# Kernel tuning notes

Measured on AMD Instinct MI355X. Metric: run time of the kernel, lower is better.

Reference implementation:

```python
import jax, jax.numpy as jnp
import numpy as np

B, T, M, D, L = 8, 4096, 32768, 128, 3  # L = ebm_GNN_layer_num - 1


def _lin(x, W, b):
    return x @ W + b


def setup_inputs() -> dict:
    key = jax.random.key(0)
    ks = jax.random.split(key, 24)
    s = 0.05
    inp = {
        "x_1st": jax.random.normal(ks[0], (B, T, 2, D), dtype=jnp.float32),
        "x_2nd": jax.random.normal(ks[1], (B, M, 4, D), dtype=jnp.float32),
        "A_causal": jax.random.uniform(ks[2], (B, 1, M), dtype=jnp.float32),
        "edge": jax.random.randint(ks[3], (2, M), 0, T, dtype=jnp.int64),
        # per-layer node/edge weights (stacked over L layers)
        "node_W": jax.random.normal(ks[4], (L, D, D)) * s,
        "node_b": jnp.zeros((L, D)),
        "mlp_W": jax.random.normal(ks[5], (L, D, D)) * s,
        "mlp_b": jnp.zeros((L, D)),
        "edgeL_W": jax.random.normal(ks[6], (L, D, D)) * s,
        "edgeL_b": jnp.zeros((L, D)),
        # node readout MLP: D -> 2D -> D -> 1
        "nro_W1": jax.random.normal(ks[7], (D, 2 * D)) * s, "nro_b1": jnp.zeros((2 * D,)),
        "nro_W2": jax.random.normal(ks[8], (2 * D, D)) * s, "nro_b2": jnp.zeros((D,)),
        "nro_W3": jax.random.normal(ks[9], (D, 1)) * s, "nro_b3": jnp.zeros((1,)),
        # edge readout MLP
        "ero_W1": jax.random.normal(ks[10], (D, 2 * D)) * s, "ero_b1": jnp.zeros((2 * D,)),
        "ero_W2": jax.random.normal(ks[11], (2 * D, D)) * s, "ero_b2": jnp.zeros((D,)),
        "ero_W3": jax.random.normal(ks[12], (D, 1)) * s, "ero_b3": jnp.zeros((1,)),
    }
    return inp


def reference(x_1st, x_2nd, A_causal, node_W, node_b, mlp_W, mlp_b,
              edgeL_W, edgeL_b, nro_W1, nro_b1, nro_W2, nro_b2, nro_W3, nro_b3,
              ero_W1, ero_b1, ero_W2, ero_b2, ero_W3, ero_b3, edge):
    ni = jnp.array([0, 0, 1, 1])  # node_i_indice
    nj = jnp.array([0, 1, 0, 1])  # node_j_indice
    e0, e1 = edge[0], edge[1]
    a = A_causal[:, 0, :, None, None]  # (B, M, 1, 1)
    xn, xe = x_1st, x_2nd
    for i in range(L):
        # --- node layer: gather -> mask-multiply -> scatter_add -> linear ---
        msg = xn[:, e1] * a                          # (B, M, 2, D)
        upd = jnp.zeros_like(xn).at[:, e0].add(msg)  # (B, T, 2, D)
        xn_new = _lin(xn + upd, node_W[i], node_b[i])
        # --- edge layer (uses updated node features, as in torch forward) ---
        ei = xn_new[:, e0][:, :, ni]                 # (B, M, 4, D)
        ej = xn_new[:, e1][:, :, nj]                 # (B, M, 4, D)
        xe_new = _lin(xe + _lin(ei + ej, mlp_W[i], mlp_b[i]), edgeL_W[i], edgeL_b[i])
        if i < L - 1:
            xn_new = jax.nn.relu(xn_new)
            xe_new = jax.nn.relu(xe_new)
        xn, xe = xn_new, xe_new
    # readouts (dropout=0, concat=False)
    h_node = _lin(jax.nn.relu(_lin(jax.nn.relu(_lin(xn, nro_W1, nro_b1)), nro_W2, nro_b2)), nro_W3, nro_b3)[..., 0]
    h_edge = _lin(jax.nn.relu(_lin(jax.nn.relu(_lin(xe, ero_W1, ero_b1)), ero_W2, ero_b2)), ero_W3, ero_b3)[..., 0]
    return h_node, h_edge  # (B,T,2), (B,M,4)
```

## Files before the change

kernel.cpp:

```cpp
#include <hip/hip_runtime.h>

#define NB 8
#define NT 4096
#define NM 32768
#define ND 128

typedef __attribute__((ext_vector_type(8))) short bf16x8;
typedef __attribute__((ext_vector_type(4))) float f32x4;
typedef __attribute__((ext_vector_type(4))) unsigned int u32x4;

#define MFMA(a,b,c) __builtin_amdgcn_mfma_f32_16x16x32_bf16(a,b,c,0,0,0)

__device__ __forceinline__ unsigned short f2bf(float x) {
  unsigned u = __float_as_uint(x);
  u += 0x7FFFu + ((u >> 16) & 1u);
  return (unsigned short)(u >> 16);
}
__device__ __forceinline__ float bf2f(unsigned short h) {
  return __uint_as_float(((unsigned)h) << 16);
}

__device__ __forceinline__ bf16x8 ldsFrag(const char* lds, int row, int kByte, int rowStride) {
  return *(const bf16x8*)(lds + ((row * rowStride + kByte) ^ ((row & 7) << 4)));
}

__global__ __launch_bounds__(256) void k_prep(
    const float* __restrict__ W, char* __restrict__ dst,
    int K, int N, int khShift, int perShift, int total)
{
  int i = blockIdx.x * 256 + threadIdx.x;
  if (i >= total) return;
  int m  = i >> perShift;
  int j  = i & ((1 << perShift) - 1);
  int n  = j >> khShift;
  int kh = j & ((1 << khShift) - 1);
  int k0 = kh << 3;
  const float* Wm = W + (size_t)m * K * N;
  char* dm = dst + (size_t)m * K * N * 2;
  unsigned short tmp[8];
  #pragma unroll
  for (int jj = 0; jj < 8; ++jj) tmp[jj] = f2bf(Wm[(k0 + jj) * N + n]);
  *(u32x4*)(dm + ((n * K * 2 + k0 * 2) ^ ((n & 7) << 4))) = *(u32x4*)tmp;
}

__global__ __launch_bounds__(256) void k_csr_count(const int* __restrict__ edge, int* deg) {
  int m = blockIdx.x * 256 + threadIdx.x;
  if (m < NM) atomicAdd(&deg[edge[m]], 1);
}
__global__ __launch_bounds__(64) void k_csr_scan(const int* __restrict__ deg,
                                                 int* __restrict__ off, int* __restrict__ cursor) {
  __shared__ int partial[64];
  int t = threadIdx.x;
  int base = t * 64;
  int sum = 0;
  for (int i = 0; i < 64; ++i) sum += deg[base + i];
  partial[t] = sum;
  __syncthreads();
  if (t == 0) {
    int run = 0;
    for (int i = 0; i < 64; ++i) { int v = partial[i]; partial[i] = run; run += v; }
  }
  __syncthreads();
  int run = partial[t];
  for (int i = 0; i < 64; ++i) {
    off[base + i] = run; cursor[base + i] = run;
    run += deg[base + i];
  }
  if (t == 63) off[NT] = NM;
}
__global__ __launch_bounds__(256) void k_csr_fill(const int* __restrict__ edge,
                                                  int* cursor, int* __restrict__ csr) {
  int m = blockIdx.x * 256 + threadIdx.x;
  if (m < NM) { int pos = atomicAdd(&cursor[edge[m]], 1); csr[pos] = m; }
}
__global__ __launch_bounds__(256) void k_csr_sort(const int* __restrict__ off, int* __restrict__ csr) {
  int n = blockIdx.x * 256 + threadIdx.x;
  if (n < NT) {
    int s = off[n], e = off[n + 1];
    for (int i = s + 1; i < e; ++i) {
      int v = csr[i]; int j = i - 1;
      while (j >= s && csr[j] > v) { csr[j + 1] = csr[j]; --j; }
      csr[j + 1] = v;
    }
  }
}

__global__ __launch_bounds__(256) void k_node(
    const float* __restrict__ xnIn, float* __restrict__ xnOut,
    const float* __restrict__ A, const int* __restrict__ edge,
    const int* __restrict__ off, const int* __restrict__ csr,
    const float* __restrict__ W, const float* __restrict__ bias, int doReluIn)
{
  __shared__ float Ws[ND * ND];
  __shared__ float xs[32][ND];
  const int t = threadIdx.x;
  for (int i = t; i < ND * ND; i += 256) Ws[i] = W[i];

  const int rowBase = blockIdx.x << 5;
  {
    const int r  = t >> 3;
    const int c0 = (t & 7) << 4;
    const int grow = rowBase + r;
    const int ch   = grow & 1;
    const int node = (grow >> 1) & (NT - 1);
    const int b    = grow >> 13;
    f32x4 acc[4];
    {
      const float4* xr = (const float4*)(xnIn + (size_t)grow * ND + c0);
      #pragma unroll
      for (int q = 0; q < 4; ++q) {
        float4 v = xr[q];
        if (doReluIn) {
          v.x = fmaxf(v.x, 0.f); v.y = fmaxf(v.y, 0.f);
          v.z = fmaxf(v.z, 0.f); v.w = fmaxf(v.w, 0.f);
        }
        acc[q] = (f32x4){v.x, v.y, v.z, v.w};
      }
    }
    const int s = off[node], e = off[node + 1];
    for (int p = s; p < e; ++p) {
      int m = csr[p];
      float a = A[b * NM + m];
      int e1 = edge[NM + m];
      const float4* src = (const float4*)(xnIn + (size_t)(((b * NT + e1) << 1) + ch) * ND + c0);
      #pragma unroll
      for (int q = 0; q < 4; ++q) {
        float4 v = src[q];
        if (doReluIn) {
          v.x = fmaxf(v.x, 0.f); v.y = fmaxf(v.y, 0.f);
          v.z = fmaxf(v.z, 0.f); v.w = fmaxf(v.w, 0.f);
        }
        acc[q][0] = fmaf(a, v.x, acc[q][0]);
        acc[q][1] = fmaf(a, v.y, acc[q][1]);
        acc[q][2] = fmaf(a, v.z, acc[q][2]);
        acc[q][3] = fmaf(a, v.w, acc[q][3]);
      }
    }
    #pragma unroll
    for (int q = 0; q < 4; ++q) *(f32x4*)&xs[r][c0 + q * 4] = acc[q];
  }
  const int c4 = (t & 31) << 2;
  const int rg = t >> 5;
  float4 bv = *(const float4*)(bias + c4);
  __syncthreads();
  float acc[4][4];
  #pragma unroll
  for (int r = 0; r < 4; ++r)
    #pragma unroll
    for (int c = 0; c < 4; ++c) acc[r][c] = 0.f;
  for (int k = 0; k < ND; k += 4) {
    float4 sv[4];
    #pragma unroll
    for (int r = 0; r < 4; ++r) sv[r] = *(const float4*)&xs[(rg << 2) + r][k];
    #pragma unroll
    for (int j = 0; j < 4; ++j) {
      float4 w = *(const float4*)&Ws[(k + j) * ND + c4];
      #pragma unroll
      for (int r = 0; r < 4; ++r) {
        float s = ((const float*)&sv[r])[j];
        acc[r][0] += s * w.x; acc[r][1] += s * w.y;
        acc[r][2] += s * w.z; acc[r][3] += s * w.w;
      }
    }
  }
  #pragma unroll
  for (int r = 0; r < 4; ++r) {
    float4 o;
    o.x = acc[r][0] + bv.x; o.y = acc[r][1] + bv.y;
    o.z = acc[r][2] + bv.z; o.w = acc[r][3] + bv.w;
    *(float4*)&xnOut[(size_t)(rowBase + (rg << 2) + r) * ND + c4] = o;
  }
}

template<int IN_F32>
__global__ __launch_bounds__(512, 4) void k_edge_mfma(
    const float* __restrict__ xn,
    const float* __restrict__ xeInF, const unsigned short* __restrict__ xeInH,
    unsigned short* xeOut,
    const int* __restrict__ edge,
    const char* __restrict__ WmImg, const float* __restrict__ bm,
    const char* __restrict__ WeImg, const float* __restrict__ be,
    int doReluOut, int nTiles)
{
  __shared__ __align__(16) char WmT[128 * 256];
  __shared__ __align__(16) char WeT[128 * 256];
  __shared__ __align__(16) char sA[64 * 256];
  const int t = threadIdx.x;
  {
    const u32x4* sm = (const u32x4*)WmImg;
    const u32x4* se = (const u32x4*)WeImg;
    u32x4* dm = (u32x4*)WmT;
    u32x4* de = (u32x4*)WeT;
    for (int i = t; i < 2048; i += 512) { dm[i] = sm[i]; de[i] = se[i]; }
  }
  const int w   = t >> 6;
  const int l   = t & 63;
  const int l15 = l & 15;
  const int lg  = l >> 4;
  const int rg2 = w >> 2;
  const int wc  = w & 3;
  float bmv[2], bev[2];
  #pragma unroll
  for (int fc = 0; fc < 2; ++fc) {
    int col = wc * 32 + fc * 16 + l15;
    bmv[fc] = bm[col];
    bev[fc] = be[col];
  }
  const int srow = t >> 3;
  __syncthreads();

  for (int tile = blockIdx.x; tile < nTiles; tile += gridDim.x) {
    const int rowBase = tile << 6;
    {
      int grow = rowBase + srow;
      int cch = grow & 3;
      int m = (grow >> 2) & (NM - 1);
      int b = grow >> 17;
      int e0 = edge[m], e1 = edge[NM + m];
      const float4* p0 = (const float4*)(xn + (size_t)((b * NT + e0) * 2 + (cch >> 1)) * ND);
      const float4* p1 = (const float4*)(xn + (size_t)((b * NT + e1) * 2 + (cch & 1)) * ND);
      #pragma unroll
      for (int hh = 0; hh < 2; ++hh) {
        int h = (t & 7) + hh * 8;
        float4 a0 = p0[h * 2], a1 = p0[h * 2 + 1];
        float4 c0 = p1[h * 2], c1 = p1[h * 2 + 1];
        unsigned short tmp[8];
        tmp[0] = f2bf(a0.x + c0.x); tmp[1] = f2bf(a0.y + c0.y);
        tmp[2] = f2bf(a0.z + c0.z); tmp[3] = f2bf(a0.w + c0.w);
        tmp[4] = f2bf(a1.x + c1.x); tmp[5] = f2bf(a1.y + c1.y);
        tmp[6] = f2bf(a1.z + c1.z); tmp[7] = f2bf(a1.w + c1.w);
        *(u32x4*)(sA + ((srow * 256 + h * 16) ^ ((srow & 7) << 4))) = *(u32x4*)tmp;
      }
    }
    float xev[2][2][4];
    #pragma unroll
    for (int fr = 0; fr < 2; ++fr)
      #pragma unroll
      for (int fc = 0; fc < 2; ++fc) {
        int col = wc * 32 + fc * 16 + l15;
        #pragma unroll
        for (int i = 0; i < 4; ++i) {
          int r = rg2 * 32 + fr * 16 + lg * 4 + i;
          size_t idx = (size_t)(rowBase + r) * ND + col;
          xev[fr][fc][i] = IN_F32 ? xeInF[idx] : bf2f(xeInH[idx]);
        }
      }
    __syncthreads();
    f32x4 acc[2][2];
    #pragma unroll
    for (int fr = 0; fr < 2; ++fr)
      #pragma unroll
      for (int fc = 0; fc < 2; ++fc) acc[fr][fc] = (f32x4){0.f, 0.f, 0.f, 0.f};
    #pragma unroll
    for (int ks = 0; ks < 4; ++ks) {
      int kb = ks * 64 + lg * 16;
      bf16x8 b0 = ldsFrag(WmT, wc * 32 + l15,      kb, 256);
      bf16x8 b1 = ldsFrag(WmT, wc * 32 + 16 + l15, kb, 256);
      #pragma unroll
      for (int fr = 0; fr < 2; ++fr) {
        bf16x8 a = ldsFrag(sA, rg2 * 32 + fr * 16 + l15, kb, 256);
        acc[fr][0] = MFMA(a, b0, acc[fr][0]);
        acc[fr][1] = MFMA(a, b1, acc[fr][1]);
      }
    }
    __syncthreads();
    #pragma unroll
    for (int fr = 0; fr < 2; ++fr)
      #pragma unroll
      for (int fc = 0; fc < 2; ++fc) {
        int col = wc * 32 + fc * 16 + l15;
        #pragma unroll
        for (int i = 0; i < 4; ++i) {
          int r = rg2 * 32 + fr * 16 + lg * 4 + i;
          float v = xev[fr][fc][i] + acc[fr][fc][i] + bmv[fc];
          *(unsigned short*)(sA + ((r * 256 + col * 2) ^ ((r & 7) << 4))) = f2bf(v);
        }
      }
    __syncthreads();
    #pragma unroll
    for (int fr = 0; fr < 2; ++fr)
      #pragma unroll
      for (int fc = 0; fc < 2; ++fc) acc[fr][fc] = (f32x4){0.f, 0.f, 0.f, 0.f};
    #pragma unroll
    for (int ks = 0; ks < 4; ++ks) {
      int kb = ks * 64 + lg * 16;
      bf16x8 b0 = ldsFrag(WeT, wc * 32 + l15,      kb, 256);
      bf16x8 b1 = ldsFrag(WeT, wc * 32 + 16 + l15, kb, 256);
      #pragma unroll
      for (int fr = 0; fr < 2; ++fr) {
        bf16x8 a = ldsFrag(sA, rg2 * 32 + fr * 16 + l15, kb, 256);
        acc[fr][0] = MFMA(a, b0, acc[fr][0]);
        acc[fr][1] = MFMA(a, b1, acc[fr][1]);
      }
    }
    __syncthreads();
    #pragma unroll
    for (int fr = 0; fr < 2; ++fr)
      #pragma unroll
      for (int fc = 0; fc < 2; ++fc) {
        int col = wc * 32 + fc * 16 + l15;
        #pragma unroll
        for (int i = 0; i < 4; ++i) {
          int r = rg2 * 32 + fr * 16 + lg * 4 + i;
          float o = acc[fr][fc][i] + bev[fc];
          if (doReluOut) o = fmaxf(o, 0.f);
          xeOut[(size_t)(rowBase + r) * ND + col] = f2bf(o);
        }
      }
  }
}

template<int INBF16>
__global__ __launch_bounds__(512, 2) void k_ro_fused(
    const float* __restrict__ inF, const unsigned short* __restrict__ inH,
    float* __restrict__ out, int nTiles,
    const char* __restrict__ W1Img, const float* __restrict__ b1,
    const char* __restrict__ W2Img, const float* __restrict__ b2,
    const float* __restrict__ W3, const float* __restrict__ b3)
{
  __shared__ __align__(16) char W1T[256 * 256];
  __shared__ __align__(16) char W2T[128 * 512];
  __shared__ __align__(16) char sA[32 * 256];
  __shared__ __align__(16) char h1[32 * 512];
  __shared__ float red[2][32][8];
  const int t = threadIdx.x;
  {
    const u32x4* s1 = (const u32x4*)W1Img;
    const u32x4* s2 = (const u32x4*)W2Img;
    u32x4* d1 = (u32x4*)W1T;
    u32x4* d2 = (u32x4*)W2T;
    for (int i = t; i < 4096; i += 512) { d1[i] = s1[i]; d2[i] = s2[i]; }
  }
  const int w   = t >> 6;
  const int l   = t & 63;
  const int l15 = l & 15;
  const int lg  = l >> 4;
  float b1v[2];
  #pragma unroll
  for (int fc = 0; fc < 2; ++fc) b1v[fc] = b1[w * 32 + fc * 16 + l15];
  const float b2v = b2[w * 16 + l15];
  const float w3v = W3[w * 16 + l15];
  const float b3v = b3[0];
  const int srow = t >> 4;
  float4 pv0, pv1;
  u32x4 pvH;
  int tile = blockIdx.x;
  if (tile < nTiles) {
    if (INBF16) {
      pvH = *(const u32x4*)((const char*)inH + (size_t)((tile << 5) + srow) * 256 + (t & 15) * 16);
    } else {
      const float4* p = (const float4*)(inF + (size_t)((tile << 5) + srow) * ND + (t & 15) * 8);
      pv0 = p[0]; pv1 = p[1];
    }
  }
  __syncthreads();

  int par = 0;
  int prevRow = -1;
  for (; tile < nTiles; tile += gridDim.x) {
    const int rowBase = tile << 5;
    {
      u32x4 vv;
      if (INBF16) {
        vv = pvH;
      } else {
        unsigned short tmp[8];
        tmp[0] = f2bf(pv0.x); tmp[1] = f2bf(pv0.y); tmp[2] = f2bf(pv0.z); tmp[3] = f2bf(pv0.w);
        tmp[4] = f2bf(pv1.x); tmp[5] = f2bf(pv1.y); tmp[6] = f2bf(pv1.z); tmp[7] = f2bf(pv1.w);
        vv = *(u32x4*)tmp;
      }
      *(u32x4*)(sA + ((srow * 256 + (t & 15) * 16) ^ ((srow & 7) << 4))) = vv;
    }
    __syncthreads();
    if (prevRow >= 0 && t < 32) {
      float s = b3v;
      #pragma unroll
      for (int q = 0; q < 8; ++q) s += red[par ^ 1][t][q];
      out[prevRow + t] = s;
    }
    {
      int nt2 = tile + (int)gridDim.x;
      if (nt2 < nTiles) {
        if (INBF16) {
          pvH = *(const u32x4*)((const char*)inH + (size_t)((nt2 << 5) + srow) * 256 + (t & 15) * 16);
        } else {
          const float4* p = (const float4*)(inF + (size_t)((nt2 << 5) + srow) * ND + (t & 15) * 8);
          pv0 = p[0]; pv1 = p[1];
        }
      }
    }
    {
      f32x4 acc[2][2];
      #pragma unroll
      for (int fr = 0; fr < 2; ++fr)
        #pragma unroll
        for (int fc = 0; fc < 2; ++fc) acc[fr][fc] = (f32x4){0.f, 0.f, 0.f, 0.f};
      #pragma unroll
      for (int ks = 0; ks < 4; ++ks) {
        int kb = ks * 64 + lg * 16;
        bf16x8 a0 = ldsFrag(sA, l15,      kb, 256);
        bf16x8 a1 = ldsFrag(sA, 16 + l15, kb, 256);
        bf16x8 b0 = ldsFrag(W1T, w * 32 + l15,      kb, 256);
        bf16x8 b1f = ldsFrag(W1T, w * 32 + 16 + l15, kb, 256);
        acc[0][0] = MFMA(a0, b0, acc[0][0]);
        acc[0][1] = MFMA(a0, b1f, acc[0][1]);
        acc[1][0] = MFMA(a1, b0, acc[1][0]);
        acc[1][1] = MFMA(a1, b1f, acc[1][1]);
      }
      __syncthreads();
      #pragma unroll
      for (int fr = 0; fr < 2; ++fr)
        #pragma unroll
        for (int fc = 0; fc < 2; ++fc) {
          int col = w * 32 + fc * 16 + l15;
          #pragma unroll
          for (int i = 0; i < 4; ++i) {
            int r = fr * 16 + lg * 4 + i;
            float o = fmaxf(acc[fr][fc][i] + b1v[fc], 0.f);
            *(unsigned short*)(h1 + ((r * 512 + col * 2) ^ ((r & 7) << 4))) = f2bf(o);
          }
        }
    }
    __syncthreads();
    {
      f32x4 acc[2];
      acc[0] = (f32x4){0.f, 0.f, 0.f, 0.f};
      acc[1] = (f32x4){0.f, 0.f, 0.f, 0.f};
      #pragma unroll
      for (int ks = 0; ks < 8; ++ks) {
        int kb = ks * 64 + lg * 16;
        bf16x8 a0 = ldsFrag(h1, l15,      kb, 512);
        bf16x8 a1 = ldsFrag(h1, 16 + l15, kb, 512);
        bf16x8 bb = ldsFrag(W2T, w * 16 + l15, kb, 512);
        acc[0] = MFMA(a0, bb, acc[0]);
        acc[1] = MFMA(a1, bb, acc[1]);
      }
      #pragma unroll
      for (int fr = 0; fr < 2; ++fr)
        #pragma unroll
        for (int i = 0; i < 4; ++i) {
          float p = fmaxf(acc[fr][i] + b2v, 0.f) * w3v;
          p += __shfl_xor(p, 1);
          p += __shfl_xor(p, 2);
          p += __shfl_xor(p, 4);
          p += __shfl_xor(p, 8);
          if (l15 == 0) red[par][fr * 16 + lg * 4 + i][w] = p;
        }
    }
    prevRow = rowBase;
    par ^= 1;
  }
  __syncthreads();
  if (prevRow >= 0 && t < 32) {
    float s = b3v;
    #pragma unroll
    for (int q = 0; q < 8; ++q) s += red[par ^ 1][t][q];
    out[prevRow + t] = s;
  }
}

extern "C" void kernel_launch(void* const* d_in, const int* in_sizes, int n_in,
                              void* d_out, int out_size, void* d_ws, size_t ws_size,
                              hipStream_t stream)
{
  const float* x1     = (const float*)d_in[0];
  const float* x2     = (const float*)d_in[1];
  const float* Ac     = (const float*)d_in[2];
  const int*   edge   = (const int*)d_in[3];
  const float* node_W = (const float*)d_in[4];
  const float* node_b = (const float*)d_in[5];
  const float* mlp_W  = (const float*)d_in[6];
  const float* mlp_b  = (const float*)d_in[7];
  const float* egL_W  = (const float*)d_in[8];
  const float* egL_b  = (const float*)d_in[9];
  const float* nro_W1 = (const float*)d_in[10];
  const float* nro_b1 = (const float*)d_in[11];
  const float* nro_W2 = (const float*)d_in[12];
  const float* nro_b2 = (const float*)d_in[13];
  const float* nro_W3 = (const float*)d_in[14];
  const float* nro_b3 = (const float*)d_in[15];
  const float* ero_W1 = (const float*)d_in[16];
  const float* ero_b1 = (const float*)d_in[17];
  const float* ero_W2 = (const float*)d_in[18];
  const float* ero_b2 = (const float*)d_in[19];
  const float* ero_W3 = (const float*)d_in[20];
  const float* ero_b3 = (const float*)d_in[21];
  float* out = (float*)d_out;

  const size_t xnElems = (size_t)NB * NT * 2 * ND;
  const size_t xeElems = (size_t)NB * NM * 4 * ND;
  const size_t wBytes  = 3 * 128 * 128 * 2 * 2
                       + 4 * (128 * 256 * 2);
  if (ws_size < xnElems * 2 * sizeof(float) + xeElems * 2 + wBytes) return;

  float* xnA = (float*)d_ws;
  float* xnB = xnA + xnElems;
  unsigned short* xeH = (unsigned short*)(xnB + xnElems);
  char*  wWm = (char*)(xeH + xeElems);
  char*  wWe = wWm + 3 * 128 * 128 * 2;
  char*  wN1 = wWe + 3 * 128 * 128 * 2;
  char*  wN2 = wN1 + 128 * 256 * 2;
  char*  wE1 = wN2 + 128 * 256 * 2;
  char*  wE2 = wE1 + 128 * 256 * 2;

  int* deg    = (int*)d_out;
  int* off    = deg + NT;
  int* cursor = off + NT + 1;
  int* csr    = cursor + NT;

  k_prep<<<24, 256, 0, stream>>>(mlp_W, wWm, 128, 128, 4, 11, 3 * 2048);
  k_prep<<<24, 256, 0, stream>>>(egL_W, wWe, 128, 128, 4, 11, 3 * 2048);
  k_prep<<<16, 256, 0, stream>>>(nro_W1, wN1, 128, 256, 4, 12, 4096);
  k_prep<<<16, 256, 0, stream>>>(nro_W2, wN2, 256, 128, 5, 12, 4096);
  k_prep<<<16, 256, 0, stream>>>(ero_W1, wE1, 128, 256, 4, 12, 4096);
  k_prep<<<16, 256, 0, stream>>>(ero_W2, wE2, 256, 128, 5, 12, 4096);

  hipMemsetAsync(deg, 0, NT * sizeof(int), stream);
  k_csr_count<<<NM / 256, 256, 0, stream>>>(edge, deg);
  k_csr_scan<<<1, 64, 0, stream>>>(deg, off, cursor);
  k_csr_fill<<<NM / 256, 256, 0, stream>>>(edge, cursor, csr);
  k_csr_sort<<<NT / 256, 256, 0, stream>>>(off, csr);

  const int eTiles = (NB * NM * 4) / 64;
  k_node<<<2048, 256, 0, stream>>>(x1, xnA, Ac, edge, off, csr, node_W, node_b, 0);
  k_edge_mfma<1><<<512, 512, 0, stream>>>(xnA, x2, nullptr, xeH, edge,
                                          wWm, mlp_b, wWe, egL_b, 1, eTiles);
  k_node<<<2048, 256, 0, stream>>>(xnA, xnB, Ac, edge, off, csr,
                                   node_W + ND * ND, node_b + ND, 1);
  k_edge_mfma<0><<<512, 512, 0, stream>>>(xnB, nullptr, xeH, xeH, edge,
                                          wWm + 128 * 128 * 2, mlp_b + ND,
                                          wWe + 128 * 128 * 2, egL_b + ND, 1, eTiles);
  k_node<<<2048, 256, 0, stream>>>(xnB, xnA, Ac, edge, off, csr,
                                   node_W + 2 * ND * ND, node_b + 2 * ND, 1);
  k_edge_mfma<0><<<512, 512, 0, stream>>>(xnA, nullptr, xeH, xeH, edge,
                                          wWm + 2 * 128 * 128 * 2, mlp_b + 2 * ND,
                                          wWe + 2 * 128 * 128 * 2, egL_b + 2 * ND, 0, eTiles);
  k_ro_fused<0><<<512, 512, 0, stream>>>(xnA, nullptr, out, (NB * NT * 2) / 32,
                                         wN1, nro_b1, wN2, nro_b2, nro_W3, nro_b3);
  k_ro_fused<1><<<512, 512, 0, stream>>>(nullptr, xeH, out + NB * NT * 2, (NB * NM * 4) / 32,
                                         wE1, ero_b1, wE2, ero_b2, ero_W3, ero_b3);
}
```

Before: 1.391 ms.

## Use bf16 MFMA in node layer and hold readout weights in registers

The node kernel's fp32 scalar 128x128 GEMM becomes a bf16 MFMA GEMM. It uses a preswizzled bf16 weight image held in LDS and a persistent tile loop, so each block loads its weights once. The readout kernels now keep W1/W2 fragments in registers instead of LDS, which frees shared memory and allows 4 blocks per CU and a grid twice as large. The cost is that node aggregates are rounded to bf16 before the linear layer, and the readout kernels carry more register pressure.

```diff
diff --git a/kernel.cpp b/kernel.cpp
--- a/kernel.cpp
+++ b/kernel.cpp
@@ -85,90 +85,113 @@
   }
 }
 
-__global__ __launch_bounds__(256) void k_node(
+__global__ __launch_bounds__(256, 4) void k_node(
     const float* __restrict__ xnIn, float* __restrict__ xnOut,
     const float* __restrict__ A, const int* __restrict__ edge,
     const int* __restrict__ off, const int* __restrict__ csr,
-    const float* __restrict__ W, const float* __restrict__ bias, int doReluIn)
+    const char* __restrict__ WImg, const float* __restrict__ bias,
+    int doReluIn, int nTiles)
 {
-  __shared__ float Ws[ND * ND];
-  __shared__ float xs[32][ND];
+  __shared__ __align__(16) char WT[128 * 256];
+  __shared__ __align__(16) char xs[32 * 256];
   const int t = threadIdx.x;
-  for (int i = t; i < ND * ND; i += 256) Ws[i] = W[i];
-
-  const int rowBase = blockIdx.x << 5;
   {
-    const int r  = t >> 3;
-    const int c0 = (t & 7) << 4;
-    const int grow = rowBase + r;
-    const int ch   = grow & 1;
-    const int node = (grow >> 1) & (NT - 1);
-    const int b    = grow >> 13;
-    f32x4 acc[4];
+    const u32x4* s = (const u32x4*)WImg;
+    u32x4* d = (u32x4*)WT;
+    for (int i = t; i < 2048; i += 256) d[i] = s[i];
+  }
+  const int w   = t >> 6;
+  const int l   = t & 63;
+  const int l15 = l & 15;
+  const int lg  = l >> 4;
+  float bv2[2];
+  #pragma unroll
+  for (int fc = 0; fc < 2; ++fc) bv2[fc] = bias[w * 32 + fc * 16 + l15];
+  const int gr = t >> 3;
+  const int c0 = (t & 7) << 4;
+  __syncthreads();
+
+  for (int tile = blockIdx.x; tile < nTiles; tile += gridDim.x) {
+    const int rowBase = tile << 5;
     {
-      const float4* xr = (const float4*)(xnIn + (size_t)grow * ND + c0);
-      #pragma unroll
-      for (int q = 0; q < 4; ++q) {
-        float4 v = xr[q];
-        if (doReluIn) {
-          v.x = fmaxf(v.x, 0.f); v.y = fmaxf(v.y, 0.f);
-          v.z = fmaxf(v.z, 0.f); v.w = fmaxf(v.w, 0.f);
-        }
-        acc[q] = (f32x4){v.x, v.y, v.z, v.w};
-      }
-    }
-    const int s = off[node], e = off[node + 1];
-    for (int p = s; p < e; ++p) {
-      int m = csr[p];
-      float a = A[b * NM + m];
-      int e1 = edge[NM + m];
-      const float4* src = (const float4*)(xnIn + (size_t)(((b * NT + e1) << 1) + ch) * ND + c0);
-      #pragma unroll
-      for (int q = 0; q < 4; ++q) {
-        float4 v = src[q];
-        if (doReluIn) {
-          v.x = fmaxf(v.x, 0.f); v.y = fmaxf(v.y, 0.f);
-          v.z = fmaxf(v.z, 0.f); v.w = fmaxf(v.w, 0.f);
-        }
-        acc[q][0] = fmaf(a, v.x, acc[q][0]);
-        acc[q][1] = fmaf(a, v.y, acc[q][1]);
-        acc[q][2] = fmaf(a, v.z, acc[q][2]);
-        acc[q][3] = fmaf(a, v.w, acc[q][3]);
-      }
-    }
-    #pragma unroll
-    for (int q = 0; q < 4; ++q) *(f32x4*)&xs[r][c0 + q * 4] = acc[q];
-  }
-  const int c4 = (t & 31) << 2;
-  const int rg = t >> 5;
-  float4 bv = *(const float4*)(bias + c4);
-  __syncthreads();
-  float acc[4][4];
-  #pragma unroll
-  for (int r = 0; r < 4; ++r)
-    #pragma unroll
-    for (int c = 0; c < 4; ++c) acc[r][c] = 0.f;
-  for (int k = 0; k < ND; k += 4) {
-    float4 sv[4];
-    #pragma unroll
-    for (int r = 0; r < 4; ++r) sv[r] = *(const float4*)&xs[(rg << 2) + r][k];
-    #pragma unroll
-    for (int j = 0; j < 4; ++j) {
-      float4 w = *(const float4*)&Ws[(k + j) * ND + c4];
-      #pragma unroll
-      for (int r = 0; r < 4; ++r) {
-        float s = ((const float*)&sv[r])[j];
-        acc[r][0] += s * w.x; acc[r][1] += s * w.y;
-        acc[r][2] += s * w.z; acc[r][3] += s * w.w;
-      }
-    }
-  }
-  #pragma unroll
-  for (int r = 0; r < 4; ++r) {
-    float4 o;
-    o.x = acc[r][0] + bv.x; o.y = acc[r][1] + bv.y;
-    o.z = acc[r][2] + bv.z; o.w = acc[r][3] + bv.w;
-    *(float4*)&xnOut[(size_t)(rowBase + (rg << 2) + r) * ND + c4] = o;
+      const int grow = rowBase + gr;
+      const int ch   = grow & 1;
+      const int node = (grow >> 1) & (NT - 1);
+      const int b    = grow >> 13;
+      f32x4 acc[4];
+      {
+        const float4* xr = (const float4*)(xnIn + (size_t)grow * ND + c0);
+        #pragma unroll
+        for (int q = 0; q < 4; ++q) {
+          float4 v = xr[q];
+          if (doReluIn) {
+            v.x = fmaxf(v.x, 0.f); v.y = fmaxf(v.y, 0.f);
+            v.z = fmaxf(v.z, 0.f); v.w = fmaxf(v.w, 0.f);
+          }
+          acc[q] = (f32x4){v.x, v.y, v.z, v.w};
+        }
+      }
+      const int s = off[node], e = off[node + 1];
+      for (int p = s; p < e; ++p) {
+        int m = csr[p];
+        float a = A[b * NM + m];
+        int e1 = edge[NM + m];
+        const float4* src = (const float4*)(xnIn + (size_t)(((b * NT + e1) << 1) + ch) * ND + c0);
+        #pragma unroll
+        for (int q = 0; q < 4; ++q) {
+          float4 v = src[q];
+          if (doReluIn) {
+            v.x = fmaxf(v.x, 0.f); v.y = fmaxf(v.y, 0.f);
+            v.z = fmaxf(v.z, 0.f); v.w = fmaxf(v.w, 0.f);
+          }
+          acc[q][0] = fmaf(a, v.x, acc[q][0]);
+          acc[q][1] = fmaf(a, v.y, acc[q][1]);
+          acc[q][2] = fmaf(a, v.z, acc[q][2]);
+          acc[q][3] = fmaf(a, v.w, acc[q][3]);
+        }
+      }
+      unsigned short tmp[8];
+      #pragma unroll
+      for (int q = 0; q < 2; ++q)
+        #pragma unroll
+        for (int j = 0; j < 4; ++j) tmp[q * 4 + j] = f2bf(acc[q][j]);
+      *(u32x4*)(xs + ((gr * 256 + c0 * 2) ^ ((gr & 7) << 4))) = *(u32x4*)tmp;
+      #pragma unroll
+      for (int q = 0; q < 2; ++q)
+        #pragma unroll
+        for (int j = 0; j < 4; ++j) tmp[q * 4 + j] = f2bf(acc[2 + q][j]);
+      *(u32x4*)(xs + ((gr * 256 + c0 * 2 + 16) ^ ((gr & 7) << 4))) = *(u32x4*)tmp;
+    }
+    __syncthreads();
+    f32x4 acc2[2][2];
+    #pragma unroll
+    for (int fr = 0; fr < 2; ++fr)
+      #pragma unroll
+      for (int fc = 0; fc < 2; ++fc) acc2[fr][fc] = (f32x4){0.f, 0.f, 0.f, 0.f};
+    #pragma unroll
+    for (int ks = 0; ks < 4; ++ks) {
+      int kb = ks * 64 + lg * 16;
+      bf16x8 b0 = ldsFrag(WT, w * 32 + l15,      kb, 256);
+      bf16x8 b1 = ldsFrag(WT, w * 32 + 16 + l15, kb, 256);
+      bf16x8 a0 = ldsFrag(xs, l15,      kb, 256);
+      bf16x8 a1 = ldsFrag(xs, 16 + l15, kb, 256);
+      acc2[0][0] = MFMA(a0, b0, acc2[0][0]);
+      acc2[0][1] = MFMA(a0, b1, acc2[0][1]);
+      acc2[1][0] = MFMA(a1, b0, acc2[1][0]);
+      acc2[1][1] = MFMA(a1, b1, acc2[1][1]);
+    }
+    __syncthreads();
+    #pragma unroll
+    for (int fr = 0; fr < 2; ++fr)
+      #pragma unroll
+      for (int fc = 0; fc < 2; ++fc) {
+        int col = w * 32 + fc * 16 + l15;
+        #pragma unroll
+        for (int i = 0; i < 4; ++i) {
+          int r = fr * 16 + lg * 4 + i;
+          xnOut[(size_t)(rowBase + r) * ND + col] = acc2[fr][fc][i] + bv2[fc];
+        }
+      }
   }
 }
 
@@ -311,30 +334,37 @@
 }
 
 template<int INBF16>
-__global__ __launch_bounds__(512, 2) void k_ro_fused(
+__global__ __launch_bounds__(512, 4) void k_ro_fused(
     const float* __restrict__ inF, const unsigned short* __restrict__ inH,
     float* __restrict__ out, int nTiles,
     const char* __restrict__ W1Img, const float* __restrict__ b1,
     const char* __restrict__ W2Img, const float* __restrict__ b2,
     const float* __restrict__ W3, const float* __restrict__ b3)
 {
-  __shared__ __align__(16) char W1T[256 * 256];
-  __shared__ __align__(16) char W2T[128 * 512];
   __shared__ __align__(16) char sA[32 * 256];
   __shared__ __align__(16) char h1[32 * 512];
   __shared__ float red[2][32][8];
   const int t = threadIdx.x;
-  {
-    const u32x4* s1 = (const u32x4*)W1Img;
-    const u32x4* s2 = (const u32x4*)W2Img;
-    u32x4* d1 = (u32x4*)W1T;
-    u32x4* d2 = (u32x4*)W2T;
-    for (int i = t; i < 4096; i += 512) { d1[i] = s1[i]; d2[i] = s2[i]; }
-  }
   const int w   = t >> 6;
   const int l   = t & 63;
   const int l15 = l & 15;
   const int lg  = l >> 4;
+  bf16x8 w1f[4][2];
+  #pragma unroll
+  for (int ks = 0; ks < 4; ++ks)
+    #pragma unroll
+    for (int fc = 0; fc < 2; ++fc) {
+      int n = w * 32 + fc * 16 + l15;
+      int kb = ks * 64 + lg * 16;
+      w1f[ks][fc] = *(const bf16x8*)(W1Img + ((n * 256 + kb) ^ ((n & 7) << 4)));
+    }
+  bf16x8 w2f[8];
+  #pragma unroll
+  for (int ks = 0; ks < 8; ++ks) {
+    int n = w * 16 + l15;
+    int kb = ks * 64 + lg * 16;
+    w2f[ks] = *(const bf16x8*)(W2Img + ((n * 512 + kb) ^ ((n & 7) << 4)));
+  }
   float b1v[2];
   #pragma unroll
   for (int fc = 0; fc < 2; ++fc) b1v[fc] = b1[w * 32 + fc * 16 + l15];
@@ -353,7 +383,6 @@
       pv0 = p[0]; pv1 = p[1];
     }
   }
-  __syncthreads();
 
   int par = 0;
   int prevRow = -1;
@@ -400,12 +429,10 @@
         int kb = ks * 64 + lg * 16;
         bf16x8 a0 = ldsFrag(sA, l15,      kb, 256);
         bf16x8 a1 = ldsFrag(sA, 16 + l15, kb, 256);
-        bf16x8 b0 = ldsFrag(W1T, w * 32 + l15,      kb, 256);
-        bf16x8 b1f = ldsFrag(W1T, w * 32 + 16 + l15, kb, 256);
-        acc[0][0] = MFMA(a0, b0, acc[0][0]);
-        acc[0][1] = MFMA(a0, b1f, acc[0][1]);
-        acc[1][0] = MFMA(a1, b0, acc[1][0]);
-        acc[1][1] = MFMA(a1, b1f, acc[1][1]);
+        acc[0][0] = MFMA(a0, w1f[ks][0], acc[0][0]);
+        acc[0][1] = MFMA(a0, w1f[ks][1], acc[0][1]);
+        acc[1][0] = MFMA(a1, w1f[ks][0], acc[1][0]);
+        acc[1][1] = MFMA(a1, w1f[ks][1], acc[1][1]);
       }
       __syncthreads();
       #pragma unroll
@@ -431,9 +458,8 @@
         int kb = ks * 64 + lg * 16;
         bf16x8 a0 = ldsFrag(h1, l15,      kb, 512);
         bf16x8 a1 = ldsFrag(h1, 16 + l15, kb, 512);
-        bf16x8 bb = ldsFrag(W2T, w * 16 + l15, kb, 512);
-        acc[0] = MFMA(a0, bb, acc[0]);
-        acc[1] = MFMA(a1, bb, acc[1]);
+        acc[0] = MFMA(a0, w2f[ks], acc[0]);
+        acc[1] = MFMA(a1, w2f[ks], acc[1]);
       }
       #pragma unroll
       for (int fr = 0; fr < 2; ++fr)
@@ -489,7 +515,7 @@
 
   const size_t xnElems = (size_t)NB * NT * 2 * ND;
   const size_t xeElems = (size_t)NB * NM * 4 * ND;
-  const size_t wBytes  = 3 * 128 * 128 * 2 * 2
+  const size_t wBytes  = 3 * 128 * 128 * 2 * 3
                        + 4 * (128 * 256 * 2);
   if (ws_size < xnElems * 2 * sizeof(float) + xeElems * 2 + wBytes) return;
 
@@ -498,7 +524,8 @@
   unsigned short* xeH = (unsigned short*)(xnB + xnElems);
   char*  wWm = (char*)(xeH + xeElems);
   char*  wWe = wWm + 3 * 128 * 128 * 2;
-  char*  wN1 = wWe + 3 * 128 * 128 * 2;
+  char*  wNd = wWe + 3 * 128 * 128 * 2;
+  char*  wN1 = wNd + 3 * 128 * 128 * 2;
   char*  wN2 = wN1 + 128 * 256 * 2;
   char*  wE1 = wN2 + 128 * 256 * 2;
   char*  wE2 = wE1 + 128 * 256 * 2;
@@ -510,6 +537,7 @@
 
   k_prep<<<24, 256, 0, stream>>>(mlp_W, wWm, 128, 128, 4, 11, 3 * 2048);
   k_prep<<<24, 256, 0, stream>>>(egL_W, wWe, 128, 128, 4, 11, 3 * 2048);
+  k_prep<<<24, 256, 0, stream>>>(node_W, wNd, 128, 128, 4, 11, 3 * 2048);
   k_prep<<<16, 256, 0, stream>>>(nro_W1, wN1, 128, 256, 4, 12, 4096);
   k_prep<<<16, 256, 0, stream>>>(nro_W2, wN2, 256, 128, 5, 12, 4096);
   k_prep<<<16, 256, 0, stream>>>(ero_W1, wE1, 128, 256, 4, 12, 4096);
@@ -522,21 +550,22 @@
   k_csr_sort<<<NT / 256, 256, 0, stream>>>(off, csr);
 
   const int eTiles = (NB * NM * 4) / 64;
-  k_node<<<2048, 256, 0, stream>>>(x1, xnA, Ac, edge, off, csr, node_W, node_b, 0);
+  const int nTilesN = (NB * NT * 2) / 32;
+  k_node<<<1024, 256, 0, stream>>>(x1, xnA, Ac, edge, off, csr, wNd, node_b, 0, nTilesN);
   k_edge_mfma<1><<<512, 512, 0, stream>>>(xnA, x2, nullptr, xeH, edge,
                                           wWm, mlp_b, wWe, egL_b, 1, eTiles);
-  k_node<<<2048, 256, 0, stream>>>(xnA, xnB, Ac, edge, off, csr,
-                                   node_W + ND * ND, node_b + ND, 1);
+  k_node<<<1024, 256, 0, stream>>>(xnA, xnB, Ac, edge, off, csr,
+                                   wNd + 128 * 128 * 2, node_b + ND, 1, nTilesN);
   k_edge_mfma<0><<<512, 512, 0, stream>>>(xnB, nullptr, xeH, xeH, edge,
                                           wWm + 128 * 128 * 2, mlp_b + ND,
                                           wWe + 128 * 128 * 2, egL_b + ND, 1, eTiles);
-  k_node<<<2048, 256, 0, stream>>>(xnB, xnA, Ac, edge, off, csr,
-                                   node_W + 2 * ND * ND, node_b + 2 * ND, 1);
+  k_node<<<1024, 256, 0, stream>>>(xnB, xnA, Ac, edge, off, csr,
+                                   wNd + 2 * 128 * 128 * 2, node_b + 2 * ND, 1, nTilesN);
   k_edge_mfma<0><<<512, 512, 0, stream>>>(xnA, nullptr, xeH, xeH, edge,
                                           wWm + 2 * 128 * 128 * 2, mlp_b + 2 * ND,
                                           wWe + 2 * 128 * 128 * 2, egL_b + 2 * ND, 0, eTiles);
-  k_ro_fused<0><<<512, 512, 0, stream>>>(xnA, nullptr, out, (NB * NT * 2) / 32,
-                                         wN1, nro_b1, wN2, nro_b2, nro_W3, nro_b3);
-  k_ro_fused<1><<<512, 512, 0, stream>>>(nullptr, xeH, out + NB * NT * 2, (NB * NM * 4) / 32,
-                                         wE1, ero_b1, wE2, ero_b2, ero_W3, ero_b3);
-}
+  k_ro_fused<0><<<1024, 512, 0, stream>>>(xnA, nullptr, out, (NB * NT * 2) / 32,
+                                          wN1, nro_b1, wN2, nro_b2, nro_W3, nro_b3);
+  k_ro_fused<1><<<1024, 512, 0, stream>>>(nullptr, xeH, out + NB * NT * 2, (NB * NM * 4) / 32,
+                                          wE1, ero_b1, wE2, ero_b2, ero_W3, ero_b3);
+}
```

New measurement: 1.290 ms. 7.3% less time.
